# Kernel tuning notes

Hardware: AMD Instinct MI355X
Metric: run time of the kernel (lower is better)

## Reference

```python
import jax, jax.numpy as jnp
import numpy as np

N, E = 50000, 800000
IN_DIM, OUT_DIM, NHEAD = 256, 64, 4
SLOPE = 0.2
BN_EPS = 1e-5


def setup_inputs() -> dict:
    key = jax.random.key(0)
    ks = jax.random.split(key, 12)
    HD = NHEAD * OUT_DIM
    s = 1.0 / np.sqrt(IN_DIM)
    inp = {
        'feat': jax.random.normal(ks[0], (N, IN_DIM), dtype=jnp.float32),
        'src': jax.random.randint(ks[1], (E,), 0, N, dtype=jnp.int32),
        'dst': jax.random.randint(ks[2], (E,), 0, N, dtype=jnp.int32),
        # GATv2Conv params (DGL: separate src/dst linear, per-head attn vector, output bias)
        'W_src': jax.random.normal(ks[3], (IN_DIM, HD), dtype=jnp.float32) * s,
        'b_src': jnp.zeros((HD,), dtype=jnp.float32),
        'W_dst': jax.random.normal(ks[4], (IN_DIM, HD), dtype=jnp.float32) * s,
        'b_dst': jnp.zeros((HD,), dtype=jnp.float32),
        'attn': jax.random.normal(ks[5], (NHEAD, OUT_DIM), dtype=jnp.float32) * (1.0 / np.sqrt(OUT_DIM)),
        'out_bias': jnp.zeros((HD,), dtype=jnp.float32),
        # trailing fc: Linear(HD -> OUT_DIM) + BatchNorm1d + LeakyReLU (dropout = identity in eval)
        'fc_W': jax.random.normal(ks[6], (HD, OUT_DIM), dtype=jnp.float32) * (1.0 / np.sqrt(HD)),
        'fc_b': jnp.zeros((OUT_DIM,), dtype=jnp.float32),
        'gamma': jnp.ones((OUT_DIM,), dtype=jnp.float32),
        'beta': jnp.zeros((OUT_DIM,), dtype=jnp.float32),
    }
    return inp


def _leaky(x):
    return jnp.where(x >= 0, x, SLOPE * x)


def reference(feat, src, dst, W_src, b_src, W_dst, b_dst, attn, out_bias, fc_W, fc_b, gamma, beta):
    H, D = NHEAD, OUT_DIM
    h_src = (feat @ W_src + b_src).reshape(N, H, D)
    h_dst = (feat @ W_dst + b_dst).reshape(N, H, D)
    # per-edge GATv2 score: attn . LeakyReLU(h_src[u] + h_dst[v])
    hs_e = h_src[src]                                   # [E,H,D]
    e = jnp.einsum('ehd,hd->eh', _leaky(hs_e + h_dst[dst]), attn)  # [E,H]
    # segment softmax over incoming edges of each dst node
    m = jax.ops.segment_max(e, dst, num_segments=N)     # [N,H]
    ex = jnp.exp(e - m[dst])
    denom = jax.ops.segment_sum(ex, dst, num_segments=N)
    a = ex / denom[dst]                                 # [E,H]
    # weighted scatter-add aggregation
    rst = jax.ops.segment_sum(a[:, :, None] * hs_e, dst, num_segments=N)  # [N,H,D]
    rst = rst + out_bias.reshape(H, D)
    # trailing fc + BatchNorm1d (batch stats) + LeakyReLU
    z = rst.reshape(N, H * D) @ fc_W + fc_b
    mu = jnp.mean(z, axis=0)
    var = jnp.var(z, axis=0)
    z = (z - mu) * jax.lax.rsqrt(var + BN_EPS) * gamma + beta
    return _leaky(z)
```

## Files before the change

kernel.cpp:

```cpp
#include <hip/hip_runtime.h>
#include <math.h>

#define N_NODES 50000
#define N_EDGES 800000
#define HD 256
#define OUT_DIM 64
#define NHEAD 4
#define SLOPE 0.2f
#define BN_EPS 1e-5f
#define LOG2E 1.4426950408889634f
#define NTILES 391
#define NGROUPS 49
#define HIST_BLOCKS 96

typedef __attribute__((ext_vector_type(8))) short short8;
typedef __attribute__((ext_vector_type(4))) float float4v;

__device__ __forceinline__ float leaky(float x) { return x >= 0.f ? x : SLOPE * x; }

__device__ __forceinline__ float bf2f(unsigned short u) {
    return __uint_as_float(((unsigned)u) << 16);
}
__device__ __forceinline__ unsigned short f2bf(float f) {
    unsigned u = __float_as_uint(f);
    unsigned r = (u + 0x7fffu + ((u >> 16) & 1u)) >> 16;
    return (unsigned short)r;
}

template <int CTRL>
__device__ __forceinline__ float ror_add(float v) {
    const int r = __builtin_amdgcn_update_dpp(0, __float_as_int(v), CTRL, 0xF, 0xF, true);
    return v + __int_as_float(r);
}
__device__ __forceinline__ float group16_sum(float v) {
    v = ror_add<0x121>(v);
    v = ror_add<0x122>(v);
    v = ror_add<0x124>(v);
    v = ror_add<0x128>(v);
    return v;
}

__global__ __launch_bounds__(256) void prep_kernel(const float* __restrict__ feat,
                                                   const float* __restrict__ W_src,
                                                   const float* __restrict__ W_dst,
                                                   const float* __restrict__ fc_W,
                                                   unsigned short* __restrict__ feat_bf,
                                                   unsigned short* __restrict__ WtS,
                                                   unsigned short* __restrict__ WtD,
                                                   unsigned short* __restrict__ WtF,
                                                   int* __restrict__ cnt2,
                                                   float* __restrict__ sums,
                                                   int* __restrict__ done) {
    const int b = blockIdx.x;
    const int t = threadIdx.x;
    if (b < 12500) {
        const int i = b * 256 + t;
        const float4 v = ((const float4*)feat)[i];
        ushort4 o;
        o.x = f2bf(v.x); o.y = f2bf(v.y); o.z = f2bf(v.z); o.w = f2bf(v.w);
        ((ushort4*)feat_bf)[i] = o;
    } else if (b < 12756) {
        const int n = b - 12500;
        WtS[(size_t)n * 256 + t] = f2bf(W_src[(size_t)t * 256 + n]);
    } else if (b < 13012) {
        const int n = b - 12756;
        WtD[(size_t)n * 256 + t] = f2bf(W_dst[(size_t)t * 256 + n]);
    } else if (b < 13076) {
        const int n = b - 13012;
        WtF[(size_t)n * 256 + t] = f2bf(fc_W[(size_t)t * 64 + n]);
    } else if (b < 13174) {
        const int i = (b - 13076) * 256 + t;
        if (i < 25000) ((int4*)cnt2)[i] = make_int4(0, 0, 0, 0);
    } else {
        if (t < 128) sums[t] = 0.f;
        if (t == 128) done[0] = 0;
    }
}

__global__ __launch_bounds__(256) void proj_kernel(const unsigned short* __restrict__ A,
                                                   const unsigned short* __restrict__ BtS,
                                                   const unsigned short* __restrict__ BtD,
                                                   const float* __restrict__ bS,
                                                   const float* __restrict__ bD,
                                                   unsigned short* __restrict__ CS,
                                                   unsigned short* __restrict__ CD,
                                                   const int* __restrict__ dst,
                                                   int* __restrict__ cnt) {
    __shared__ unsigned short Bs[64 * 256];

    if (blockIdx.x < HIST_BLOCKS) {
        for (int i = blockIdx.x * 256 + threadIdx.x; i < N_EDGES; i += HIST_BLOCKS * 256)
            atomicAdd(&cnt[dst[i]], 1);
        return;
    }

    const int jid  = blockIdx.x - HIST_BLOCKS;
    const int tile = (jid >> 4) * 8 + (jid & 7);
    if (tile >= NTILES) return;
    const bool isD = ((jid >> 3) & 1) != 0;

    const int t    = threadIdx.x;
    const int w    = t >> 6;
    const int lane = t & 63;
    const int q    = lane >> 4;
    const int l16  = lane & 15;

    const unsigned short* Bt   = isD ? BtD : BtS;
    const float*          bias = isD ? bD  : bS;
    unsigned short*       C    = isD ? CD  : CS;

    const int m0 = tile * 128;

    int ar0 = m0 + w * 32 + l16;
    int ar1 = ar0 + 16;
    if (ar0 > N_NODES - 1) ar0 = N_NODES - 1;
    if (ar1 > N_NODES - 1) ar1 = N_NODES - 1;
    const unsigned short* Ab0 = A + (size_t)ar0 * 256 + q * 8;
    const unsigned short* Ab1 = A + (size_t)ar1 * 256 + q * 8;
    short8 afr0[8], afr1[8];
#pragma unroll
    for (int kk = 0; kk < 8; ++kk) {
        afr0[kk] = *(const short8*)(Ab0 + kk * 32);
        afr1[kk] = *(const short8*)(Ab1 + kk * 32);
    }

    const int r   = t >> 2;
    const int seg = t & 3;
    const int cc  = r >> 4;
    const int L   = r & 15;

    const int la8 = lane * 8;
    const int lsw[4] = {la8, la8 ^ 16, la8 ^ 32, la8 ^ 48};

    for (int ph = 0; ph < 4; ++ph) {
        const int c0 = ph * 64;

        __syncthreads();
        {
            const unsigned short* g = Bt + (size_t)(c0 + r) * 256 + seg * 64;
#pragma unroll
            for (int kk2 = 0; kk2 < 2; ++kk2) {
                const int kk   = seg * 2 + kk2;
                const int c8kk = cc * 8 + kk;
                const int key  = ((c8kk >> 1) & 3) << 4;
#pragma unroll
                for (int q2 = 0; q2 < 4; ++q2)
                    *(short8*)(&Bs[((c8kk * 64 + q2 * 16 + L) * 8) ^ key]) =
                        *(const short8*)(g + kk2 * 32 + q2 * 8);
            }
        }
        __syncthreads();

        float vb[4];
#pragma unroll
        for (int c = 0; c < 4; ++c) vb[c] = bias[c0 + c * 16 + l16];

        float4v a0[4] = {}, a1[4] = {};
#pragma unroll
        for (int kk = 0; kk < 8; ++kk) {
            const short8 af0 = afr0[kk];
            const short8 af1 = afr1[kk];
#pragma unroll
            for (int c = 0; c < 4; ++c) {
                const int c8kk = c * 8 + kk;
                const short8 b = *(const short8*)(&Bs[c8kk * 512 + lsw[(c8kk >> 1) & 3]]);
                a0[c] = __builtin_amdgcn_mfma_f32_16x16x32_bf16(af0, b, a0[c], 0, 0, 0);
                a1[c] = __builtin_amdgcn_mfma_f32_16x16x32_bf16(af1, b, a1[c], 0, 0, 0);
            }
        }

        __syncthreads();
        unsigned short* Cw = Bs + w * 2304;
#pragma unroll
        for (int c = 0; c < 4; ++c) {
            const int cl = c * 16 + l16;
#pragma unroll
            for (int i = 0; i < 4; ++i) {
                Cw[(q * 4 + i) * 72 + cl]      = f2bf(a0[c][i] + vb[c]);
                Cw[(q * 4 + i + 16) * 72 + cl] = f2bf(a1[c][i] + vb[c]);
            }
        }
#pragma unroll
        for (int j = 0; j < 4; ++j) {
            const int rl = j * 8 + (lane >> 3);
            const short8 v = *(const short8*)(Cw + rl * 72 + (lane & 7) * 8);
            const int rg = m0 + w * 32 + rl;
            if (rg < N_NODES)
                *(short8*)(&C[(size_t)rg * 256 + c0 + (lane & 7) * 8]) = v;
        }
    }
}

__global__ __launch_bounds__(256) void fc_bn_kernel(const unsigned short* __restrict__ A,
                                                    const unsigned short* __restrict__ Bt,
                                                    const float* __restrict__ bias,
                                                    float* __restrict__ C,
                                                    float* __restrict__ sums,
                                                    int M) {
    const int w    = threadIdx.x >> 6;
    const int lane = threadIdx.x & 63;
    const int q    = lane >> 4;
    const int l16  = lane & 15;
    const int m0   = blockIdx.x * 64;
    const int t    = threadIdx.x;

    __shared__ float ssum[64], ssq[64];
    if (t < 64) { ssum[t] = 0.f; ssq[t] = 0.f; }

    int arow = m0 + w * 16 + l16;
    if (arow > M - 1) arow = M - 1;
    const unsigned short* Ab  = A  + (size_t)arow * 256 + q * 8;
    const unsigned short* Btb = Bt + (size_t)l16 * 256 + q * 8;

    float4v acc[4] = {};

    for (int k0 = 0; k0 < 256; k0 += 32) {
        const short8 af = *(const short8*)(Ab + k0);
#pragma unroll
        for (int c = 0; c < 4; ++c) {
            const short8 bf = *(const short8*)(Btb + (size_t)c * 16 * 256 + k0);
            acc[c] = __builtin_amdgcn_mfma_f32_16x16x32_bf16(af, bf, acc[c], 0, 0, 0);
        }
    }
    __syncthreads();

#pragma unroll
    for (int c = 0; c < 4; ++c) {
        const int col = c * 16 + l16;
        const float b = bias[col];
        float s = 0.f, qq = 0.f;
#pragma unroll
        for (int i = 0; i < 4; ++i) {
            const int r = m0 + w * 16 + q * 4 + i;
            if (r < M) {
                const float v = acc[c][i] + b;
                C[(size_t)r * 64 + col] = v;
                s += v;
                qq += v * v;
            }
        }
        atomicAdd(&ssum[col], s);
        atomicAdd(&ssq[col], qq);
    }
    __syncthreads();
    if (t < 64) {
        atomicAdd(&sums[t], ssum[t]);
        atomicAdd(&sums[64 + t], ssq[t]);
    }
}

__global__ __launch_bounds__(512) void scan_kernel(const int* __restrict__ cnt,
                                                   int* __restrict__ offs,
                                                   int* __restrict__ bsum,
                                                   int* __restrict__ bpre,
                                                   int* __restrict__ done) {
    __shared__ int s[512];
    __shared__ bool amLast;
    const int t = threadIdx.x;
    const int i = blockIdx.x * 512 + t;
    const int v = (i < N_NODES) ? cnt[i] : 0;
    s[t] = v;
    __syncthreads();
    for (int off = 1; off < 512; off <<= 1) {
        const int x = (t >= off) ? s[t - off] : 0;
        __syncthreads();
        s[t] += x;
        __syncthreads();
    }
    if (i < N_NODES) offs[i] = s[t] - v;
    if (t == 511) {
        bsum[blockIdx.x] = s[511];
        __threadfence();
        amLast = (atomicAdd(done, 1) == (int)gridDim.x - 1);
    }
    __syncthreads();
    if (amLast) {
        const int v2 = (t < (int)gridDim.x) ? atomicAdd(&bsum[t], 0) : 0;
        s[t] = v2;
        __syncthreads();
        for (int off = 1; off < 512; off <<= 1) {
            const int x = (t >= off) ? s[t - off] : 0;
            __syncthreads();
            s[t] += x;
            __syncthreads();
        }
        if (t < (int)gridDim.x) bpre[t] = s[t] - v2;
    }
}

__global__ void scatter_kernel(const int* __restrict__ src,
                               const int* __restrict__ dst,
                               const int* __restrict__ offs,
                               const int* __restrict__ bpre,
                               int* __restrict__ cursor,
                               int* __restrict__ srcl) {
    const int i = blockIdx.x * 256 + threadIdx.x;
    if (i < N_EDGES) {
        const int d = dst[i];
        const int p = offs[d] + bpre[d >> 9] + atomicAdd(&cursor[d], 1);
        srcl[p] = src[i];
    }
}

__global__ __launch_bounds__(256) void agg_fused_kernel(const unsigned short* __restrict__ h_src,
                                                        const unsigned short* __restrict__ h_dst,
                                                        const int* __restrict__ srcl,
                                                        const int* __restrict__ offs,
                                                        const int* __restrict__ bpre,
                                                        const float* __restrict__ attn,
                                                        const float* __restrict__ out_bias,
                                                        unsigned short* __restrict__ rst) {
    const int node = blockIdx.x * 4 + (threadIdx.x >> 6);
    const int lane = threadIdx.x & 63;
    const int d4 = lane * 4;

    const int beg = offs[node] + bpre[node >> 9];
    const int end = (node + 1 == N_NODES) ? N_EDGES
                                          : (offs[node + 1] + bpre[(node + 1) >> 9]);

    const uint2 hdu = *(const uint2*)(h_dst + (size_t)node * 256 + d4);
    const float hd0 = __uint_as_float(hdu.x << 16);
    const float hd1 = __uint_as_float(hdu.x & 0xffff0000u);
    const float hd2 = __uint_as_float(hdu.y << 16);
    const float hd3 = __uint_as_float(hdu.y & 0xffff0000u);

    const float4 araw = *(const float4*)(attn + d4);
    const float c10 = araw.x * (0.6f * LOG2E), c20 = araw.x * (0.4f * LOG2E);
    const float c11 = araw.y * (0.6f * LOG2E), c21 = araw.y * (0.4f * LOG2E);
    const float c12 = araw.z * (0.6f * LOG2E), c22 = araw.z * (0.4f * LOG2E);
    const float c13 = araw.w * (0.6f * LOG2E), c23 = araw.w * (0.4f * LOG2E);

    float wsum = 0.f, a0 = 0.f, a1 = 0.f, a2 = 0.f, a3 = 0.f;

#define EDGE_BODY(sreg)                                                          \
    {                                                                            \
        const unsigned short* row = h_src + (size_t)(sreg) * 256;                \
        const uint2 u = *(const uint2*)(row + d4);                               \
        const float r0 = __uint_as_float(u.x << 16);                             \
        const float r1 = __uint_as_float(u.x & 0xffff0000u);                     \
        const float r2 = __uint_as_float(u.y << 16);                             \
        const float r3 = __uint_as_float(u.y & 0xffff0000u);                     \
        const float y0 = r0 + hd0, y1 = r1 + hd1, y2 = r2 + hd2, y3 = r3 + hd3;  \
        float pp = fmaf(c10, y0, c20 * __builtin_fabsf(y0));                     \
        pp = fmaf(c11, y1, fmaf(c21, __builtin_fabsf(y1), pp));                  \
        pp = fmaf(c12, y2, fmaf(c22, __builtin_fabsf(y2), pp));                  \
        pp = fmaf(c13, y3, fmaf(c23, __builtin_fabsf(y3), pp));                  \
        pp = group16_sum(pp);                                                    \
        const float wg = __builtin_amdgcn_exp2f(pp);                             \
        wsum += wg;                                                              \
        a0 = fmaf(wg, r0, a0);                                                   \
        a1 = fmaf(wg, r1, a1);                                                   \
        a2 = fmaf(wg, r2, a2);                                                   \
        a3 = fmaf(wg, r3, a3);                                                   \
    }

    int p = beg;
    const int nfull = (end - beg) >> 2;
    for (int it = 0; it < nfull; ++it, p += 4) {
        const int s0 = __builtin_amdgcn_readfirstlane(srcl[p]);
        const int s1 = __builtin_amdgcn_readfirstlane(srcl[p + 1]);
        const int s2 = __builtin_amdgcn_readfirstlane(srcl[p + 2]);
        const int s3 = __builtin_amdgcn_readfirstlane(srcl[p + 3]);
        EDGE_BODY(s0);
        EDGE_BODY(s1);
        EDGE_BODY(s2);
        EDGE_BODY(s3);
    }
    for (; p < end; ++p) {
        const int s0 = __builtin_amdgcn_readfirstlane(srcl[p]);
        EDGE_BODY(s0);
    }
#undef EDGE_BODY

    const float inv = (wsum > 0.f) ? 1.f / wsum : 0.f;
    const float4 ob = *(const float4*)(out_bias + d4);
    ushort4 o;
    o.x = f2bf(fmaf(a0, inv, ob.x));
    o.y = f2bf(fmaf(a1, inv, ob.y));
    o.z = f2bf(fmaf(a2, inv, ob.z));
    o.w = f2bf(fmaf(a3, inv, ob.w));
    *(ushort4*)(rst + (size_t)node * 256 + d4) = o;
}

__global__ __launch_bounds__(256) void bn_final_kernel(float* __restrict__ z,
                                                       const float* __restrict__ sums,
                                                       const float* __restrict__ gamma,
                                                       const float* __restrict__ beta) {
    const int i = blockIdx.x * 256 + threadIdx.x;
    if (i < N_NODES * 16) {
        const int c4 = (i & 15) * 4;
        float4 v = ((const float4*)z)[i];
        float out[4] = {v.x, v.y, v.z, v.w};
#pragma unroll
        for (int j = 0; j < 4; ++j) {
            const int col = c4 + j;
            const float mu  = sums[col] * (1.f / N_NODES);
            const float var = sums[64 + col] * (1.f / N_NODES) - mu * mu;
            const float sc  = rsqrtf(var + BN_EPS) * gamma[col];
            const float sh  = beta[col] - mu * sc;
            out[j] = leaky(fmaf(out[j], sc, sh));
        }
        ((float4*)z)[i] = make_float4(out[0], out[1], out[2], out[3]);
    }
}

extern "C" void kernel_launch(void* const* d_in, const int* in_sizes, int n_in,
                              void* d_out, int out_size, void* d_ws, size_t ws_size,
                              hipStream_t stream) {
    const float* feat    = (const float*)d_in[0];
    const int*   src     = (const int*)  d_in[1];
    const int*   dst     = (const int*)  d_in[2];
    const float* W_src   = (const float*)d_in[3];
    const float* b_src   = (const float*)d_in[4];
    const float* W_dst   = (const float*)d_in[5];
    const float* b_dst   = (const float*)d_in[6];
    const float* attn    = (const float*)d_in[7];
    const float* out_bias= (const float*)d_in[8];
    const float* fc_W    = (const float*)d_in[9];
    const float* fc_b    = (const float*)d_in[10];
    const float* gamma   = (const float*)d_in[11];
    const float* beta    = (const float*)d_in[12];
    float* z = (float*)d_out;

    char* ws = (char*)d_ws;
    size_t off = 0;
    auto carve = [&](size_t bytes) -> void* {
        void* p = ws + off;
        off = (off + bytes + 255) & ~(size_t)255;
        return p;
    };
    unsigned short* feat_bf = (unsigned short*)carve((size_t)N_NODES * 256 * 2);
    unsigned short* h_src_bf= (unsigned short*)carve((size_t)N_NODES * 256 * 2);
    unsigned short* h_dst_bf= (unsigned short*)carve((size_t)N_NODES * 256 * 2);
    unsigned short* rst_bf  = (unsigned short*)carve((size_t)N_NODES * 256 * 2);
    unsigned short* WtS     = (unsigned short*)carve((size_t)256 * 256 * 2);
    unsigned short* WtD     = (unsigned short*)carve((size_t)256 * 256 * 2);
    unsigned short* WtF     = (unsigned short*)carve((size_t)64 * 256 * 2);
    int*   srcl   = (int*)  carve((size_t)N_EDGES * 4);
    int*   cnt    = (int*)  carve((size_t)2 * N_NODES * 4);
    int*   cursor = cnt + N_NODES;
    int*   offs   = (int*)  carve((size_t)(N_NODES + 1) * 4);
    int*   bsum   = (int*)  carve(128 * 4);
    int*   bpre   = (int*)  carve(128 * 4);
    float* sums   = (float*)carve(128 * 4);
    int*   done   = (int*)  carve(64);

    const int nchunks = (N_NODES + 511) / 512;

    prep_kernel<<<13175, 256, 0, stream>>>(feat, W_src, W_dst, fc_W,
                                           feat_bf, WtS, WtD, WtF, cnt, sums, done);

    proj_kernel<<<HIST_BLOCKS + NGROUPS * 16, 256, 0, stream>>>(
        feat_bf, WtS, WtD, b_src, b_dst, h_src_bf, h_dst_bf, dst, cnt);

    scan_kernel<<<nchunks, 512, 0, stream>>>(cnt, offs, bsum, bpre, done);
    scatter_kernel<<<(N_EDGES + 255) / 256, 256, 0, stream>>>(src, dst, offs, bpre, cursor, srcl);

    agg_fused_kernel<<<N_NODES / 4, 256, 0, stream>>>(h_src_bf, h_dst_bf, srcl, offs, bpre,
                                                      attn, out_bias, rst_bf);

    fc_bn_kernel<<<(N_NODES + 63) / 64, 256, 0, stream>>>(rst_bf, WtF, fc_b, z, sums, N_NODES);

    bn_final_kernel<<<(N_NODES * 16 + 255) / 256, 256, 0, stream>>>(z, sums, gamma, beta);
}
```

Before: 311.8 us.

## Fuse feature bf16 conversion into projection GEMM and compute both projections per tile

The projection kernel now reads the fp32 features directly and packs them to bf16 in registers, so the separate conversion pass and its intermediate feat_bf buffer are gone. Each block also computes both the src and dst projections for its 128-row tile by looping over 8 column phases, instead of one projection per block. This removes a full read-and-write pass over the feature matrix and halves the A-fragment loads. The cost is half as many GEMM blocks (391), each doing twice the work, which lowers parallelism on a large GPU, and double the fp32 bytes read per A fragment.

```diff
diff --git a/kernel.cpp b/kernel.cpp
--- a/kernel.cpp
+++ b/kernel.cpp
@@ -10,7 +10,6 @@
 #define BN_EPS 1e-5f
 #define LOG2E 1.4426950408889634f
 #define NTILES 391
-#define NGROUPS 49
 #define HIST_BLOCKS 96
 
 typedef __attribute__((ext_vector_type(8))) short short8;
@@ -25,6 +24,15 @@
     unsigned u = __float_as_uint(f);
     unsigned r = (u + 0x7fffu + ((u >> 16) & 1u)) >> 16;
     return (unsigned short)r;
+}
+
+__device__ __forceinline__ short8 pack8(const float4 a, const float4 b) {
+    short8 r;
+    r[0] = (short)f2bf(a.x); r[1] = (short)f2bf(a.y);
+    r[2] = (short)f2bf(a.z); r[3] = (short)f2bf(a.w);
+    r[4] = (short)f2bf(b.x); r[5] = (short)f2bf(b.y);
+    r[6] = (short)f2bf(b.z); r[7] = (short)f2bf(b.w);
+    return r;
 }
 
 template <int CTRL>
@@ -40,11 +48,9 @@
     return v;
 }
 
-__global__ __launch_bounds__(256) void prep_kernel(const float* __restrict__ feat,
-                                                   const float* __restrict__ W_src,
+__global__ __launch_bounds__(256) void prep_kernel(const float* __restrict__ W_src,
                                                    const float* __restrict__ W_dst,
                                                    const float* __restrict__ fc_W,
-                                                   unsigned short* __restrict__ feat_bf,
                                                    unsigned short* __restrict__ WtS,
                                                    unsigned short* __restrict__ WtD,
                                                    unsigned short* __restrict__ WtF,
@@ -53,23 +59,16 @@
                                                    int* __restrict__ done) {
     const int b = blockIdx.x;
     const int t = threadIdx.x;
-    if (b < 12500) {
-        const int i = b * 256 + t;
-        const float4 v = ((const float4*)feat)[i];
-        ushort4 o;
-        o.x = f2bf(v.x); o.y = f2bf(v.y); o.z = f2bf(v.z); o.w = f2bf(v.w);
-        ((ushort4*)feat_bf)[i] = o;
-    } else if (b < 12756) {
-        const int n = b - 12500;
-        WtS[(size_t)n * 256 + t] = f2bf(W_src[(size_t)t * 256 + n]);
-    } else if (b < 13012) {
-        const int n = b - 12756;
+    if (b < 256) {
+        WtS[(size_t)b * 256 + t] = f2bf(W_src[(size_t)t * 256 + b]);
+    } else if (b < 512) {
+        const int n = b - 256;
         WtD[(size_t)n * 256 + t] = f2bf(W_dst[(size_t)t * 256 + n]);
-    } else if (b < 13076) {
-        const int n = b - 13012;
+    } else if (b < 576) {
+        const int n = b - 512;
         WtF[(size_t)n * 256 + t] = f2bf(fc_W[(size_t)t * 64 + n]);
-    } else if (b < 13174) {
-        const int i = (b - 13076) * 256 + t;
+    } else if (b < 674) {
+        const int i = (b - 576) * 256 + t;
         if (i < 25000) ((int4*)cnt2)[i] = make_int4(0, 0, 0, 0);
     } else {
         if (t < 128) sums[t] = 0.f;
@@ -77,7 +76,7 @@
     }
 }
 
-__global__ __launch_bounds__(256) void proj_kernel(const unsigned short* __restrict__ A,
+__global__ __launch_bounds__(256) void proj_kernel(const float* __restrict__ feat,
                                                    const unsigned short* __restrict__ BtS,
                                                    const unsigned short* __restrict__ BtD,
                                                    const float* __restrict__ bS,
@@ -94,10 +93,8 @@
         return;
     }
 
-    const int jid  = blockIdx.x - HIST_BLOCKS;
-    const int tile = (jid >> 4) * 8 + (jid & 7);
+    const int tile = blockIdx.x - HIST_BLOCKS;
     if (tile >= NTILES) return;
-    const bool isD = ((jid >> 3) & 1) != 0;
 
     const int t    = threadIdx.x;
     const int w    = t >> 6;
@@ -105,23 +102,23 @@
     const int q    = lane >> 4;
     const int l16  = lane & 15;
 
-    const unsigned short* Bt   = isD ? BtD : BtS;
-    const float*          bias = isD ? bD  : bS;
-    unsigned short*       C    = isD ? CD  : CS;
-
     const int m0 = tile * 128;
 
     int ar0 = m0 + w * 32 + l16;
     int ar1 = ar0 + 16;
     if (ar0 > N_NODES - 1) ar0 = N_NODES - 1;
     if (ar1 > N_NODES - 1) ar1 = N_NODES - 1;
-    const unsigned short* Ab0 = A + (size_t)ar0 * 256 + q * 8;
-    const unsigned short* Ab1 = A + (size_t)ar1 * 256 + q * 8;
+    const float* Af0 = feat + (size_t)ar0 * 256 + q * 8;
+    const float* Af1 = feat + (size_t)ar1 * 256 + q * 8;
     short8 afr0[8], afr1[8];
 #pragma unroll
     for (int kk = 0; kk < 8; ++kk) {
-        afr0[kk] = *(const short8*)(Ab0 + kk * 32);
-        afr1[kk] = *(const short8*)(Ab1 + kk * 32);
+        const float4 x0 = *(const float4*)(Af0 + kk * 32);
+        const float4 y0 = *(const float4*)(Af0 + kk * 32 + 4);
+        const float4 x1 = *(const float4*)(Af1 + kk * 32);
+        const float4 y1 = *(const float4*)(Af1 + kk * 32 + 4);
+        afr0[kk] = pack8(x0, y0);
+        afr1[kk] = pack8(x1, y1);
     }
 
     const int r   = t >> 2;
@@ -132,8 +129,12 @@
     const int la8 = lane * 8;
     const int lsw[4] = {la8, la8 ^ 16, la8 ^ 32, la8 ^ 48};
 
-    for (int ph = 0; ph < 4; ++ph) {
-        const int c0 = ph * 64;
+    for (int ph = 0; ph < 8; ++ph) {
+        const bool isD = (ph >= 4);
+        const int  c0  = (ph & 3) * 64;
+        const unsigned short* Bt   = isD ? BtD : BtS;
+        const float*          bias = isD ? bD  : bS;
+        unsigned short*       C    = isD ? CD  : CS;
 
         __syncthreads();
         {
@@ -429,7 +430,6 @@
         off = (off + bytes + 255) & ~(size_t)255;
         return p;
     };
-    unsigned short* feat_bf = (unsigned short*)carve((size_t)N_NODES * 256 * 2);
     unsigned short* h_src_bf= (unsigned short*)carve((size_t)N_NODES * 256 * 2);
     unsigned short* h_dst_bf= (unsigned short*)carve((size_t)N_NODES * 256 * 2);
     unsigned short* rst_bf  = (unsigned short*)carve((size_t)N_NODES * 256 * 2);
@@ -447,11 +447,11 @@
 
     const int nchunks = (N_NODES + 511) / 512;
 
-    prep_kernel<<<13175, 256, 0, stream>>>(feat, W_src, W_dst, fc_W,
-                                           feat_bf, WtS, WtD, WtF, cnt, sums, done);
-
-    proj_kernel<<<HIST_BLOCKS + NGROUPS * 16, 256, 0, stream>>>(
-        feat_bf, WtS, WtD, b_src, b_dst, h_src_bf, h_dst_bf, dst, cnt);
+    prep_kernel<<<675, 256, 0, stream>>>(W_src, W_dst, fc_W,
+                                         WtS, WtD, WtF, cnt, sums, done);
+
+    proj_kernel<<<HIST_BLOCKS + NTILES, 256, 0, stream>>>(
+        feat, WtS, WtD, b_src, b_dst, h_src_bf, h_dst_bf, dst, cnt);
 
     scan_kernel<<<nchunks, 512, 0, stream>>>(cnt, offs, bsum, bpre, done);
     scatter_kernel<<<(N_EDGES + 255) / 256, 256, 0, stream>>>(src, dst, offs, bpre, cursor, srcl);
```

Measured after the change: 311.6 us. About the same (-0.1%).
